# Optimization experiments

Hardware: AMD Instinct MI355X
Metric: run time of the kernel (lower is better)

Reference implementation:

```python
import jax, jax.numpy as jnp
import numpy as np

N, D, K, ITERS = 500000, 64, 256, 10


def setup_inputs() -> dict:
    key = jax.random.key(0)
    k1, k2 = jax.random.split(key)
    x = jax.random.normal(k1, (N, D), dtype=jnp.float32)
    init_idx = jax.random.randint(k2, (K,), 0, N, dtype=jnp.int32)
    return {"x": x, "init_idx": init_idx, "n_clusters": K, "n_iters": ITERS}


def _lloyd_step(x, x_sq, centroids):
    dists = x_sq[:, None] - 2.0 * (x @ centroids.T) + jnp.sum(centroids * centroids, axis=1)[None, :]
    assign = jnp.argmin(dists, axis=1)                       # [N]
    sums = jax.ops.segment_sum(x, assign, num_segments=centroids.shape[0])   # [K, D]
    counts = jax.ops.segment_sum(jnp.ones((x.shape[0],), x.dtype), assign,
                                 num_segments=centroids.shape[0])            # [K]
    new_c = sums / jnp.maximum(counts, 1.0)[:, None]
    # empty clusters keep their previous centroid (sklearn relocates; carry-over is the standard Lloyd fallback)
    return jnp.where(counts[:, None] > 0, new_c, centroids)


def reference(x, init_idx, n_clusters, n_iters):
    # original: x.detach() -> no gradient flows through k-means
    x = jax.lax.stop_gradient(x)
    x_sq = jnp.sum(x * x, axis=1)  # [N], reused every iteration
    centroids0 = x[init_idx]       # [K, D] random-point init

    def body(c, _):
        return _lloyd_step(x, x_sq, c), None

    centroids, _ = jax.lax.scan(body, centroids0, None, length=n_iters)
    return centroids  # cluster_centers_ [K, D]
```

## Files before the change

### kernel.cpp

```cpp
#include <hip/hip_runtime.h>


#define D 64
#define K 256
#define ITERS 10
#define BLOCK 1024
#define NB_MAX 256
#define EPS 2e-3f
#define SPAD 66
#define PART_STRIDE (K * D + K)
#define SMEM_BYTES (32768 * 2 + (256 + 256 * SPAD + 256) * 4)

typedef __attribute__((ext_vector_type(8))) short bf16x8;
typedef __attribute__((ext_vector_type(4))) float f32x4;
typedef __attribute__((ext_vector_type(4))) short short4v;

__device__ __forceinline__ unsigned short f2bf(float f) {
    unsigned u = __builtin_bit_cast(unsigned, f);
    u = u + 0x7FFFu + ((u >> 16) & 1u);
    return (unsigned short)(u >> 16);
}
__device__ __forceinline__ float bf2f(unsigned short h) {
    unsigned u = ((unsigned)h) << 16;
    return __builtin_bit_cast(float, u);
}

__global__ void init_gather(const float* __restrict__ x,
                            const int* __restrict__ idx,
                            float* __restrict__ cent,
                            float* __restrict__ csq) {
    int k = blockIdx.x;
    int d = threadIdx.x;
    float v = x[(size_t)idx[k] * D + d];
    cent[k * D + d] = v;
    float s = v * v;
    #pragma unroll
    for (int off = 32; off > 0; off >>= 1) s += __shfl_down(s, off);
    if (d == 0) csq[k] = s;
}

__device__ __forceinline__ int resolve_bk(
        const f32x4 (&acc)[16], const float* __restrict__ s_csq,
        const float* __restrict__ cent, const float* __restrict__ xr,
        int g4) {
    float gmin = 3.4e38f;
    int gidx = 0;
    #pragma unroll
    for (int t = 0; t < 16; ++t) {
        f32x4 q = *(const f32x4*)&s_csq[t * 16 + (g4 << 2)];
        #pragma unroll
        for (int r = 0; r < 4; ++r) {
            float sc = acc[t][r] + q[r];
            int m = t * 16 + (g4 << 2) + r;
            if (sc < gmin) { gmin = sc; gidx = m; }
        }
    }
    #pragma unroll
    for (int off = 16; off <= 32; off <<= 1) {
        float so = __shfl_xor(gmin, off);
        int io = __shfl_xor(gidx, off);
        if (so < gmin || (so == gmin && io < gidx)) { gmin = so; gidx = io; }
    }
    unsigned long long cmask = 0;
    #pragma unroll
    for (int t = 0; t < 16; ++t) {
        f32x4 q = *(const f32x4*)&s_csq[t * 16 + (g4 << 2)];
        #pragma unroll
        for (int r = 0; r < 4; ++r) {
            float sc = acc[t][r] + q[r];
            if (sc <= gmin + EPS) cmask |= 1ull << (t * 4 + r);
        }
    }
    int nb_ = __popcll(cmask);
    nb_ += __shfl_xor(nb_, 16);
    nb_ += __shfl_xor(nb_, 32);

    int bk = gidx;
    if (__any(nb_ >= 2)) {
        float xsq = 0.0f;
        #pragma unroll
        for (int d = 0; d < D; ++d) xsq += xr[d] * xr[d];
        float eb = 3.4e38f;
        int em = 0x7fffffff;
        unsigned long long mm = cmask;
        while (mm) {
            int b = __ffsll((unsigned long long)mm) - 1;
            mm &= mm - 1;
            int m = ((b >> 2) << 4) + (g4 << 2) + (b & 3);
            const float* cr = cent + m * D;
            float dot = 0.0f;
            #pragma unroll
            for (int d4 = 0; d4 < D; d4 += 4) {
                float4 c4 = *(const float4*)(cr + d4);
                dot += c4.x * xr[d4 + 0];
                dot += c4.y * xr[d4 + 1];
                dot += c4.z * xr[d4 + 2];
                dot += c4.w * xr[d4 + 3];
            }
            float es = xsq - 2.0f * dot + s_csq[m];
            if (es < eb || (es == eb && m < em)) { eb = es; em = m; }
        }
        #pragma unroll
        for (int off = 16; off <= 32; off <<= 1) {
            float so = __shfl_xor(eb, off);
            int io = __shfl_xor(em, off);
            if (so < eb || (so == eb && io < em)) { eb = so; em = io; }
        }
        bk = em;
    }
    return bk;
}

__global__ __launch_bounds__(BLOCK, 4) void assign_mfma(
        const float* __restrict__ x,
        const float* __restrict__ cent,
        const float* __restrict__ csq_g,
        float* __restrict__ parts,
        int N, int ppb) {
    extern __shared__ char smem[];
    short* chi = (short*)smem;
    short* clo = chi + 16384;
    float* s_csq = (float*)(clo + 16384);
    float* s_sums = s_csq + 256;
    float* s_cnt = s_sums + 256 * SPAD;

    const int tid = threadIdx.x;

    for (int i = tid; i < (K * D) / 4; i += BLOCK) {
        float4 c4 = ((const float4*)cent)[i];
        int elem = i * 4;
        int m = elem >> 6;
        int k0 = elem & 63;
        int g = k0 >> 3, e0 = k0 & 7;
        float cv[4] = {c4.x, c4.y, c4.z, c4.w};
        short4v hv, lv;
        #pragma unroll
        for (int j = 0; j < 4; ++j) {
            float v = -2.0f * cv[j];
            unsigned short h = f2bf(v);
            hv[j] = (short)h;
            lv[j] = (short)f2bf(v - bf2f(h));
        }
        int dst = (g * 256 + m) * 8 + e0;
        *(short4v*)&chi[dst] = hv;
        *(short4v*)&clo[dst] = lv;
    }
    if (tid < K) s_csq[tid] = csq_g[tid];
    for (int i = tid; i < 256 * SPAD; i += BLOCK) s_sums[i] = 0.0f;
    if (tid < K) s_cnt[tid] = 0.0f;
    __syncthreads();

    const int wv = tid >> 6;
    const int lane = tid & 63;
    const int c15 = lane & 15;
    const int g4 = lane >> 4;

    const int base = blockIdx.x * ppb;
    int lim = base + ppb;
    if (lim > N) lim = N;
    const int ngroups = (lim > base) ? ((lim - base + 15) >> 4) : 0;

    #pragma unroll 1
    for (int g0 = wv; g0 < ngroups; g0 += 16) {
        int prow = base + g0 * 16 + c15;
        const bool vA = prow < lim;
        const float* xr = x + (size_t)(vA ? prow : (lim - 1)) * D;

        float xf[16];
        bf16x8 bh[2], bl[2];
        #pragma unroll
        for (int s = 0; s < 2; ++s) {
            const float4* pa = (const float4*)(xr + s * 32 + g4 * 8);
            float4 a0 = pa[0], a1 = pa[1];
            xf[s * 8 + 0] = a0.x; xf[s * 8 + 1] = a0.y;
            xf[s * 8 + 2] = a0.z; xf[s * 8 + 3] = a0.w;
            xf[s * 8 + 4] = a1.x; xf[s * 8 + 5] = a1.y;
            xf[s * 8 + 6] = a1.z; xf[s * 8 + 7] = a1.w;
        }
        #pragma unroll
        for (int s = 0; s < 2; ++s) {
            #pragma unroll
            for (int e = 0; e < 8; ++e) {
                float va = xf[s * 8 + e];
                unsigned short ha = f2bf(va);
                bh[s][e] = (short)ha;
                bl[s][e] = (short)f2bf(va - bf2f(ha));
            }
        }

        f32x4 acc[16];
        #pragma unroll
        for (int t = 0; t < 16; ++t) {
            f32x4 z = {0.f, 0.f, 0.f, 0.f};
            acc[t] = z;
            #pragma unroll
            for (int s = 0; s < 2; ++s) {
                int ai = (((s * 4 + g4) * 256) + t * 16 + c15) * 8;
                bf16x8 ah = *(const bf16x8*)&chi[ai];
                bf16x8 al = *(const bf16x8*)&clo[ai];
                acc[t] = __builtin_amdgcn_mfma_f32_16x16x32_bf16(ah, bh[s], acc[t], 0, 0, 0);
                acc[t] = __builtin_amdgcn_mfma_f32_16x16x32_bf16(ah, bl[s], acc[t], 0, 0, 0);
                acc[t] = __builtin_amdgcn_mfma_f32_16x16x32_bf16(al, bh[s], acc[t], 0, 0, 0);
            }
        }

        int bk = resolve_bk(acc, s_csq, cent, xr, g4);
        if (vA) {
            #pragma unroll
            for (int s = 0; s < 2; ++s) {
                #pragma unroll
                for (int e = 0; e < 8; ++e)
                    atomicAdd(&s_sums[bk * SPAD + s * 32 + g4 * 8 + e],
                              xf[s * 8 + e]);
            }
            if (g4 == 0) atomicAdd(&s_cnt[bk], 1.0f);
        }
    }

    __syncthreads();
    float* part = parts + (size_t)blockIdx.x * PART_STRIDE;
    for (int i = tid; i < K * D; i += BLOCK) {
        int k = i >> 6, d = i & 63;
        part[i] = s_sums[k * SPAD + d];
    }
    if (tid < K) part[K * D + tid] = s_cnt[tid];
}

__global__ void finalize2(float* __restrict__ cent,
                          const float* __restrict__ parts,
                          float* __restrict__ csq_g,
                          int nb) {
    __shared__ float tmp[4][64];
    __shared__ float tcnt[4];
    int k = blockIdx.x;
    int sl = threadIdx.x >> 6;
    int d = threadIdx.x & 63;
    float s = 0.0f, c = 0.0f;
    for (int b = sl; b < nb; b += 4) {
        const float* pb = parts + (size_t)b * PART_STRIDE;
        s += pb[k * D + d];
        c += pb[K * D + k];
    }
    tmp[sl][d] = s;
    if (d == 0) tcnt[sl] = c;
    __syncthreads();
    if (sl == 0) {
        float st = tmp[0][d] + tmp[1][d] + tmp[2][d] + tmp[3][d];
        float ct = tcnt[0] + tcnt[1] + tcnt[2] + tcnt[3];
        float oldc = cent[k * D + d];
        float nc = (ct > 0.0f) ? (st / ct) : oldc;
        cent[k * D + d] = nc;
        float v = nc * nc;
        #pragma unroll
        for (int off = 32; off > 0; off >>= 1) v += __shfl_down(v, off);
        if (d == 0) csq_g[k] = v;
    }
}

extern "C" void kernel_launch(void* const* d_in, const int* in_sizes, int n_in,
                              void* d_out, int out_size, void* d_ws, size_t ws_size,
                              hipStream_t stream) {
    const float* x = (const float*)d_in[0];
    const int* init_idx = (const int*)d_in[1];

    int N = in_sizes[0] / D;

    float* cent = (float*)d_out;

    int nb = NB_MAX;
    size_t need = ((size_t)NB_MAX * PART_STRIDE + K) * sizeof(float);
    if (ws_size < need) {
        size_t avail = (ws_size > (size_t)K * sizeof(float))
                           ? ws_size - (size_t)K * sizeof(float) : 0;
        nb = (int)(avail / (PART_STRIDE * sizeof(float)));
        if (nb < 1) nb = 1;
    }
    float* parts = (float*)d_ws;
    float* csq = parts + (size_t)nb * PART_STRIDE;

    hipFuncSetAttribute(reinterpret_cast<const void*>(assign_mfma),
                        hipFuncAttributeMaxDynamicSharedMemorySize, SMEM_BYTES);

    init_gather<<<dim3(K), dim3(64), 0, stream>>>(x, init_idx, cent, csq);

    int ppb = (N + nb - 1) / nb;
    for (int it = 0; it < ITERS; ++it) {
        assign_mfma<<<dim3(nb), dim3(BLOCK), SMEM_BYTES, stream>>>(
            x, cent, csq, parts, N, ppb);
        finalize2<<<dim3(K), dim3(256), 0, stream>>>(cent, parts, csq, nb);
    }
}
```

Baseline: 2.374 ms.

## Split assignment and accumulation into separate kernels with a labels buffer

The fused assign+accumulate kernel is split into an MFMA assignment kernel that writes per-point labels and a separate accumulation kernel that re-reads x and labels to build per-block partial sums in shared memory. Block size drops to 512 and the partial count rises to 512, with finalize widened to reduce 8 slices. The intent is to cut each kernel's LDS and register footprint so more blocks fit per CU. The cost is a second full read of x each iteration plus label traffic.

```diff
diff --git a/kernel.cpp b/kernel.cpp
--- a/kernel.cpp
+++ b/kernel.cpp
@@ -4,12 +4,14 @@
 #define D 64
 #define K 256
 #define ITERS 10
-#define BLOCK 1024
-#define NB_MAX 256
+#define BLOCK 512
+#define GRID_A 512
+#define NB_MAX 512
 #define EPS 2e-3f
 #define SPAD 66
 #define PART_STRIDE (K * D + K)
-#define SMEM_BYTES (32768 * 2 + (256 + 256 * SPAD + 256) * 4)
+#define SMEM_A (32768 * 2 + 256 * 4)
+#define SMEM_C ((256 * SPAD + 256) * 4)
 
 typedef __attribute__((ext_vector_type(8))) short bf16x8;
 typedef __attribute__((ext_vector_type(4))) float f32x4;
@@ -39,90 +41,16 @@
     if (d == 0) csq[k] = s;
 }
 
-__device__ __forceinline__ int resolve_bk(
-        const f32x4 (&acc)[16], const float* __restrict__ s_csq,
-        const float* __restrict__ cent, const float* __restrict__ xr,
-        int g4) {
-    float gmin = 3.4e38f;
-    int gidx = 0;
-    #pragma unroll
-    for (int t = 0; t < 16; ++t) {
-        f32x4 q = *(const f32x4*)&s_csq[t * 16 + (g4 << 2)];
-        #pragma unroll
-        for (int r = 0; r < 4; ++r) {
-            float sc = acc[t][r] + q[r];
-            int m = t * 16 + (g4 << 2) + r;
-            if (sc < gmin) { gmin = sc; gidx = m; }
-        }
-    }
-    #pragma unroll
-    for (int off = 16; off <= 32; off <<= 1) {
-        float so = __shfl_xor(gmin, off);
-        int io = __shfl_xor(gidx, off);
-        if (so < gmin || (so == gmin && io < gidx)) { gmin = so; gidx = io; }
-    }
-    unsigned long long cmask = 0;
-    #pragma unroll
-    for (int t = 0; t < 16; ++t) {
-        f32x4 q = *(const f32x4*)&s_csq[t * 16 + (g4 << 2)];
-        #pragma unroll
-        for (int r = 0; r < 4; ++r) {
-            float sc = acc[t][r] + q[r];
-            if (sc <= gmin + EPS) cmask |= 1ull << (t * 4 + r);
-        }
-    }
-    int nb_ = __popcll(cmask);
-    nb_ += __shfl_xor(nb_, 16);
-    nb_ += __shfl_xor(nb_, 32);
-
-    int bk = gidx;
-    if (__any(nb_ >= 2)) {
-        float xsq = 0.0f;
-        #pragma unroll
-        for (int d = 0; d < D; ++d) xsq += xr[d] * xr[d];
-        float eb = 3.4e38f;
-        int em = 0x7fffffff;
-        unsigned long long mm = cmask;
-        while (mm) {
-            int b = __ffsll((unsigned long long)mm) - 1;
-            mm &= mm - 1;
-            int m = ((b >> 2) << 4) + (g4 << 2) + (b & 3);
-            const float* cr = cent + m * D;
-            float dot = 0.0f;
-            #pragma unroll
-            for (int d4 = 0; d4 < D; d4 += 4) {
-                float4 c4 = *(const float4*)(cr + d4);
-                dot += c4.x * xr[d4 + 0];
-                dot += c4.y * xr[d4 + 1];
-                dot += c4.z * xr[d4 + 2];
-                dot += c4.w * xr[d4 + 3];
-            }
-            float es = xsq - 2.0f * dot + s_csq[m];
-            if (es < eb || (es == eb && m < em)) { eb = es; em = m; }
-        }
-        #pragma unroll
-        for (int off = 16; off <= 32; off <<= 1) {
-            float so = __shfl_xor(eb, off);
-            int io = __shfl_xor(em, off);
-            if (so < eb || (so == eb && io < em)) { eb = so; em = io; }
-        }
-        bk = em;
-    }
-    return bk;
-}
-
-__global__ __launch_bounds__(BLOCK, 4) void assign_mfma(
+__global__ __launch_bounds__(BLOCK, 2) void assign_mfma(
         const float* __restrict__ x,
         const float* __restrict__ cent,
         const float* __restrict__ csq_g,
-        float* __restrict__ parts,
+        int* __restrict__ labels,
         int N, int ppb) {
     extern __shared__ char smem[];
     short* chi = (short*)smem;
     short* clo = chi + 16384;
     float* s_csq = (float*)(clo + 16384);
-    float* s_sums = s_csq + 256;
-    float* s_cnt = s_sums + 256 * SPAD;
 
     const int tid = threadIdx.x;
 
@@ -146,8 +74,6 @@
         *(short4v*)&clo[dst] = lv;
     }
     if (tid < K) s_csq[tid] = csq_g[tid];
-    for (int i = tid; i < 256 * SPAD; i += BLOCK) s_sums[i] = 0.0f;
-    if (tid < K) s_cnt[tid] = 0.0f;
     __syncthreads();
 
     const int wv = tid >> 6;
@@ -161,30 +87,22 @@
     const int ngroups = (lim > base) ? ((lim - base + 15) >> 4) : 0;
 
     #pragma unroll 1
-    for (int g0 = wv; g0 < ngroups; g0 += 16) {
+    for (int g0 = wv; g0 < ngroups; g0 += 8) {
         int prow = base + g0 * 16 + c15;
         const bool vA = prow < lim;
         const float* xr = x + (size_t)(vA ? prow : (lim - 1)) * D;
 
-        float xf[16];
         bf16x8 bh[2], bl[2];
         #pragma unroll
         for (int s = 0; s < 2; ++s) {
             const float4* pa = (const float4*)(xr + s * 32 + g4 * 8);
             float4 a0 = pa[0], a1 = pa[1];
-            xf[s * 8 + 0] = a0.x; xf[s * 8 + 1] = a0.y;
-            xf[s * 8 + 2] = a0.z; xf[s * 8 + 3] = a0.w;
-            xf[s * 8 + 4] = a1.x; xf[s * 8 + 5] = a1.y;
-            xf[s * 8 + 6] = a1.z; xf[s * 8 + 7] = a1.w;
-        }
-        #pragma unroll
-        for (int s = 0; s < 2; ++s) {
+            float xv[8] = {a0.x, a0.y, a0.z, a0.w, a1.x, a1.y, a1.z, a1.w};
             #pragma unroll
             for (int e = 0; e < 8; ++e) {
-                float va = xf[s * 8 + e];
-                unsigned short ha = f2bf(va);
-                bh[s][e] = (short)ha;
-                bl[s][e] = (short)f2bf(va - bf2f(ha));
+                unsigned short h = f2bf(xv[e]);
+                bh[s][e] = (short)h;
+                bl[s][e] = (short)f2bf(xv[e] - bf2f(h));
             }
         }
 
@@ -204,15 +122,123 @@
             }
         }
 
-        int bk = resolve_bk(acc, s_csq, cent, xr, g4);
+        float gmin = 3.4e38f;
+        int gidx = 0;
+        #pragma unroll
+        for (int t = 0; t < 16; ++t) {
+            f32x4 q = *(const f32x4*)&s_csq[t * 16 + (g4 << 2)];
+            #pragma unroll
+            for (int r = 0; r < 4; ++r) {
+                float sc = acc[t][r] + q[r];
+                int m = t * 16 + (g4 << 2) + r;
+                if (sc < gmin) { gmin = sc; gidx = m; }
+            }
+        }
+        #pragma unroll
+        for (int off = 16; off <= 32; off <<= 1) {
+            float so = __shfl_xor(gmin, off);
+            int io = __shfl_xor(gidx, off);
+            if (so < gmin || (so == gmin && io < gidx)) { gmin = so; gidx = io; }
+        }
+        unsigned long long cmask = 0;
+        #pragma unroll
+        for (int t = 0; t < 16; ++t) {
+            f32x4 q = *(const f32x4*)&s_csq[t * 16 + (g4 << 2)];
+            #pragma unroll
+            for (int r = 0; r < 4; ++r) {
+                float sc = acc[t][r] + q[r];
+                if (sc <= gmin + EPS) cmask |= 1ull << (t * 4 + r);
+            }
+        }
+        int nb_ = __popcll(cmask);
+        nb_ += __shfl_xor(nb_, 16);
+        nb_ += __shfl_xor(nb_, 32);
+
+        int bk = gidx;
+        if (__any(nb_ >= 2)) {
+            float xsq = 0.0f;
+            #pragma unroll
+            for (int d = 0; d < D; ++d) xsq += xr[d] * xr[d];
+            float eb = 3.4e38f;
+            int em = 0x7fffffff;
+            unsigned long long mm = cmask;
+            while (mm) {
+                int b = __ffsll((unsigned long long)mm) - 1;
+                mm &= mm - 1;
+                int m = ((b >> 2) << 4) + (g4 << 2) + (b & 3);
+                const float* cr = cent + m * D;
+                float dot = 0.0f;
+                #pragma unroll
+                for (int d4 = 0; d4 < D; d4 += 4) {
+                    float4 c4 = *(const float4*)(cr + d4);
+                    dot += c4.x * xr[d4 + 0];
+                    dot += c4.y * xr[d4 + 1];
+                    dot += c4.z * xr[d4 + 2];
+                    dot += c4.w * xr[d4 + 3];
+                }
+                float es = xsq - 2.0f * dot + s_csq[m];
+                if (es < eb || (es == eb && m < em)) { eb = es; em = m; }
+            }
+            #pragma unroll
+            for (int off = 16; off <= 32; off <<= 1) {
+                float so = __shfl_xor(eb, off);
+                int io = __shfl_xor(em, off);
+                if (so < eb || (so == eb && io < em)) { eb = so; em = io; }
+            }
+            bk = em;
+        }
+
+        if (g4 == 0 && vA) labels[prow] = bk;
+    }
+}
+
+__global__ __launch_bounds__(BLOCK, 2) void accum(
+        const float* __restrict__ x,
+        const int* __restrict__ labels,
+        float* __restrict__ parts,
+        int N, int ppb) {
+    extern __shared__ char smem[];
+    float* s_sums = (float*)smem;
+    float* s_cnt = s_sums + 256 * SPAD;
+
+    const int tid = threadIdx.x;
+    for (int i = tid; i < 256 * SPAD; i += BLOCK) s_sums[i] = 0.0f;
+    if (tid < K) s_cnt[tid] = 0.0f;
+    __syncthreads();
+
+    const int wv = tid >> 6;
+    const int lane = tid & 63;
+    const int c15 = lane & 15;
+    const int g4 = lane >> 4;
+
+    const int base = blockIdx.x * ppb;
+    int lim = base + ppb;
+    if (lim > N) lim = N;
+    const int ngroups = (lim > base) ? ((lim - base + 15) >> 4) : 0;
+
+    #pragma unroll 1
+    for (int g0 = wv; g0 < ngroups; g0 += 8) {
+        int prow = base + g0 * 16 + c15;
+        const bool vA = prow < lim;
+        int pr = vA ? prow : (lim - 1);
+        const float* xr = x + (size_t)pr * D;
+        int bk = labels[pr];
+
+        float4 t0 = *(const float4*)(xr + g4 * 8);
+        float4 t1 = *(const float4*)(xr + g4 * 8 + 4);
+        float4 t2 = *(const float4*)(xr + 32 + g4 * 8);
+        float4 t3 = *(const float4*)(xr + 32 + g4 * 8 + 4);
+
         if (vA) {
-            #pragma unroll
-            for (int s = 0; s < 2; ++s) {
-                #pragma unroll
-                for (int e = 0; e < 8; ++e)
-                    atomicAdd(&s_sums[bk * SPAD + s * 32 + g4 * 8 + e],
-                              xf[s * 8 + e]);
-            }
+            float* row = &s_sums[bk * SPAD + g4 * 8];
+            atomicAdd(&row[0], t0.x); atomicAdd(&row[1], t0.y);
+            atomicAdd(&row[2], t0.z); atomicAdd(&row[3], t0.w);
+            atomicAdd(&row[4], t1.x); atomicAdd(&row[5], t1.y);
+            atomicAdd(&row[6], t1.z); atomicAdd(&row[7], t1.w);
+            atomicAdd(&row[32], t2.x); atomicAdd(&row[33], t2.y);
+            atomicAdd(&row[34], t2.z); atomicAdd(&row[35], t2.w);
+            atomicAdd(&row[36], t3.x); atomicAdd(&row[37], t3.y);
+            atomicAdd(&row[38], t3.z); atomicAdd(&row[39], t3.w);
             if (g4 == 0) atomicAdd(&s_cnt[bk], 1.0f);
         }
     }
@@ -230,13 +256,13 @@
                           const float* __restrict__ parts,
                           float* __restrict__ csq_g,
                           int nb) {
-    __shared__ float tmp[4][64];
-    __shared__ float tcnt[4];
+    __shared__ float tmp[8][64];
+    __shared__ float tcnt[8];
     int k = blockIdx.x;
     int sl = threadIdx.x >> 6;
     int d = threadIdx.x & 63;
     float s = 0.0f, c = 0.0f;
-    for (int b = sl; b < nb; b += 4) {
+    for (int b = sl; b < nb; b += 8) {
         const float* pb = parts + (size_t)b * PART_STRIDE;
         s += pb[k * D + d];
         c += pb[K * D + k];
@@ -245,8 +271,9 @@
     if (d == 0) tcnt[sl] = c;
     __syncthreads();
     if (sl == 0) {
-        float st = tmp[0][d] + tmp[1][d] + tmp[2][d] + tmp[3][d];
-        float ct = tcnt[0] + tcnt[1] + tcnt[2] + tcnt[3];
+        float st = 0.0f, ct = 0.0f;
+        #pragma unroll
+        for (int j = 0; j < 8; ++j) { st += tmp[j][d]; ct += tcnt[j]; }
         float oldc = cent[k * D + d];
         float nc = (ct > 0.0f) ? (st / ct) : oldc;
         cent[k * D + d] = nc;
@@ -267,26 +294,34 @@
 
     float* cent = (float*)d_out;
 
+    size_t lab_f = (size_t)((N + 3) & ~3);
     int nb = NB_MAX;
-    size_t need = ((size_t)NB_MAX * PART_STRIDE + K) * sizeof(float);
+    size_t need = (lab_f + (size_t)NB_MAX * PART_STRIDE + K) * 4;
     if (ws_size < need) {
-        size_t avail = (ws_size > (size_t)K * sizeof(float))
-                           ? ws_size - (size_t)K * sizeof(float) : 0;
-        nb = (int)(avail / (PART_STRIDE * sizeof(float)));
+        size_t avail4 = ws_size / 4;
+        size_t fixed = lab_f + K;
+        size_t rem = (avail4 > fixed) ? (avail4 - fixed) : 0;
+        nb = (int)(rem / PART_STRIDE);
         if (nb < 1) nb = 1;
     }
-    float* parts = (float*)d_ws;
+    int* labels = (int*)d_ws;
+    float* parts = (float*)d_ws + lab_f;
     float* csq = parts + (size_t)nb * PART_STRIDE;
 
     hipFuncSetAttribute(reinterpret_cast<const void*>(assign_mfma),
-                        hipFuncAttributeMaxDynamicSharedMemorySize, SMEM_BYTES);
+                        hipFuncAttributeMaxDynamicSharedMemorySize, SMEM_A);
+    hipFuncSetAttribute(reinterpret_cast<const void*>(accum),
+                        hipFuncAttributeMaxDynamicSharedMemorySize, SMEM_C);
 
     init_gather<<<dim3(K), dim3(64), 0, stream>>>(x, init_idx, cent, csq);
 
-    int ppb = (N + nb - 1) / nb;
+    int ppbA = (N + GRID_A - 1) / GRID_A;
+    int ppbC = (N + nb - 1) / nb;
     for (int it = 0; it < ITERS; ++it) {
-        assign_mfma<<<dim3(nb), dim3(BLOCK), SMEM_BYTES, stream>>>(
-            x, cent, csq, parts, N, ppb);
-        finalize2<<<dim3(K), dim3(256), 0, stream>>>(cent, parts, csq, nb);
-    }
-}
+        assign_mfma<<<dim3(GRID_A), dim3(BLOCK), SMEM_A, stream>>>(
+            x, cent, csq, labels, N, ppbA);
+        accum<<<dim3(nb), dim3(BLOCK), SMEM_C, stream>>>(
+            x, labels, parts, N, ppbC);
+        finalize2<<<dim3(K), dim3(512), 0, stream>>>(cent, parts, csq, nb);
+    }
+}
```

After: 5.614 ms. +136.5%, slower.
